# Kernel tuning notes

Hardware: AMD Instinct MI355X
Metric: run time of the kernel (lower is better)

Reference implementation:

```python
import jax, jax.numpy as jnp
import numpy as np

WH, WW = 4, 4
N_TOK = WH * WW  # 16
NUM_HEADS = 8
DIM = 96
HEAD_DIM = DIM // NUM_HEADS
SCALE = HEAD_DIM ** -0.5


def _relative_position_index():
    # Faithful to TF: tf.meshgrid default indexing='xy' (same as np.meshgrid default)
    coords = np.stack(np.meshgrid(np.arange(WH), np.arange(WW)))  # [2, WW, WH]
    flat = coords.reshape(2, -1)                                   # [2, N]
    rel = flat[:, :, None] - flat[:, None, :]                      # [2, N, N]
    rel = rel.transpose(1, 2, 0) + np.array([WH - 1, WW - 1])
    rel = rel * np.array([2 * WW - 1, 1])
    return jnp.asarray(rel.sum(-1), dtype=jnp.int32)               # [N, N]

REL_IDX = _relative_position_index()


def setup_inputs() -> dict:
    key = jax.random.key(0)
    ks = jax.random.split(key, 7)
    B, L = 16, 3136
    return {
        "x": jax.random.normal(ks[0], (B, L, N_TOK, DIM), jnp.float32),
        "mask": jax.random.normal(ks[1], (L, N_TOK, N_TOK), jnp.float32),
        "qkv_kernel": jax.random.normal(ks[2], (DIM, 3 * DIM), jnp.float32) * 0.02,
        "qkv_bias": jax.random.normal(ks[3], (3 * DIM,), jnp.float32) * 0.02,
        "proj_kernel": jax.random.normal(ks[4], (DIM, DIM), jnp.float32) * 0.02,
        "proj_bias": jax.random.normal(ks[5], (DIM,), jnp.float32) * 0.02,
        "bias_table": jax.random.normal(ks[6], (49, NUM_HEADS), jnp.float32) * 0.02,
    }


def reference(x, mask, qkv_kernel, qkv_bias, proj_kernel, proj_bias, bias_table):
    B, L, N, C = x.shape
    H, D = NUM_HEADS, HEAD_DIM
    qkv = x @ qkv_kernel + qkv_bias                      # [B, L, N, 3C]
    qkv = qkv.reshape(B * L, N, 3, H, D).transpose(2, 0, 3, 1, 4)  # [3, BL, H, N, D]
    q, k, v = qkv[0], qkv[1], qkv[2]
    attn = jnp.einsum('whid,whjd->whij', q * SCALE, k)   # [BL, H, N, N]
    rel_bias = bias_table[REL_IDX.reshape(-1)].reshape(N, N, H).transpose(2, 0, 1)  # [H, N, N]
    attn = attn + rel_bias
    attn = attn.reshape(B, L, H, N, N) + mask[:, None, :, :]        # broadcast over B, heads
    attn = jax.nn.softmax(attn.reshape(B * L, H, N, N), axis=-1)
    out = jnp.einsum('whij,whjd->whid', attn, v)         # [BL, H, N, D]
    out = out.transpose(0, 2, 1, 3).reshape(B, L, N, C)
    return out @ proj_kernel + proj_bias
```

## Files before the change

kernel.cpp:

```cpp
#include <hip/hip_runtime.h>


typedef __attribute__((ext_vector_type(4))) float f32x4;
typedef __attribute__((ext_vector_type(8))) short s16x8;
typedef __attribute__((ext_vector_type(4))) short s16x4;

#define DEV __device__ __forceinline__

DEV short f2bf(float f) {
    union { float f; unsigned int i; } v; v.f = f;
    unsigned int u = v.i;
    u += 0x7FFFu + ((u >> 16) & 1u);
    return (short)(u >> 16);
}
DEV void lds_fence() { asm volatile("s_waitcnt lgkmcnt(0)" ::: "memory"); }

#define LOG2E  1.4426950408889634f
#define QSCALE (0.2886751345948129f * 1.4426950408889634f)
#define LBASE  3136
#define WIN_PER_WAVE 49

#define WQ_OFF   0
#define WQ_SZ    (96*288*2)
#define ZP_OFF   WQ_SZ
#define WAVE_BASE (WQ_SZ + 64)
#define PW_Q     0
#define PW_K     4352
#define PW_V     8704
#define PW_A     13312
#define PW_O     23552
#define PW_STRIDE 26880
#define SMEM_TOTAL (WAVE_BASE + 4*PW_STRIDE)

#define MFMA(a,b,c) __builtin_amdgcn_mfma_f32_16x16x32_bf16((a),(b),(c),0,0,0)

__global__ __launch_bounds__(256, 1)
void winattn_kernel(const float* __restrict__ x,
                    const float* __restrict__ mask,
                    const float* __restrict__ qkvK,
                    const float* __restrict__ qkvB,
                    const float* __restrict__ projK,
                    const float* __restrict__ projB,
                    const float* __restrict__ biasT,
                    float* __restrict__ out)
{
    extern __shared__ __align__(16) char smem[];
    const int tid    = threadIdx.x;
    const int lane   = tid & 63;
    const int waveid = tid >> 6;
    const int mi     = lane & 15;
    const int g      = lane >> 4;

    for (int i = tid; i < SMEM_TOTAL/4; i += 256)
        ((unsigned int*)smem)[i] = 0u;
    __syncthreads();

    for (int e = tid; e < 96*288; e += 256) {
        int k = e / 288, n = e % 288;
        int t = n >> 4, mr = n & 15;
        int kt = k >> 5, gg = (k >> 3) & 3, jj = k & 7;
        int gs = gg ^ ((mr >> 1) & 3);
        int off = (t*3 + kt)*512 + mr*32 + gs*8 + jj;
        ((unsigned short*)(smem + WQ_OFF))[off] = (unsigned short)f2bf(qkvK[e]);
    }
    __syncthreads();

    char* wbuf = smem + WAVE_BASE + waveid*PW_STRIDE;
    const char* zp = smem + ZP_OFF;

    s16x8 wp[6][3];
#pragma unroll
    for (int t = 0; t < 6; ++t)
#pragma unroll
        for (int kt = 0; kt < 3; ++kt) {
            s16x8 v;
#pragma unroll
            for (int jj = 0; jj < 8; ++jj)
                v[jj] = f2bf(projK[(kt*32 + g*8 + jj)*96 + t*16 + mi]);
            wp[t][kt] = v;
        }
    f32x4 qb[12];
#pragma unroll
    for (int t = 0; t < 12; ++t) {
        f32x4 v;
#pragma unroll
        for (int r = 0; r < 4; ++r) v[r] = qkvB[t*16 + g*4 + r];
        qb[t] = v;
    }
    float vbias[6];
#pragma unroll
    for (int t = 0; t < 6; ++t) vbias[t] = qkvB[192 + t*16 + mi];
    f32x4 pb[6];
#pragma unroll
    for (int t = 0; t < 6; ++t) {
        f32x4 v;
#pragma unroll
        for (int r = 0; r < 4; ++r) v[r] = projB[t*16 + g*4 + r];
        pb[t] = v;
    }
    f32x4 rb[8];
#pragma unroll
    for (int h = 0; h < 8; ++h) {
        f32x4 v;
#pragma unroll
        for (int r = 0; r < 4; ++r) {
            int i = mi, j = g*4 + r;
            int idx = ((i & 3) - (j & 3) + 3)*7 + ((i >> 2) - (j >> 2) + 3);
            v[r] = biasT[idx*8 + h] * LOG2E;
        }
        rb[h] = v;
    }
    unsigned qkoff[6], voff[6];
#pragma unroll
    for (int t = 0; t < 6; ++t) {
        int f0 = t*16 + g*4;
        qkoff[t] = (unsigned)(mi*272 + (f0/12)*32 + (f0%12)*2);
        int f3 = t*16 + mi;
        voff[t]  = (unsigned)((f3/12)*576 + (f3%12)*48 + g*8);
    }
    const unsigned lane_woff = (unsigned)(mi*64 + ((g ^ ((mi >> 1) & 3)) * 16));

    const int wave_global = blockIdx.x*4 + waveid;
    const int w0 = wave_global * WIN_PER_WAVE;

    f32x4 xa[3], xb[3], mraw;
    {
        const float* xw = x + w0*1536;
#pragma unroll
        for (int kt = 0; kt < 3; ++kt) {
            xa[kt] = *(const f32x4*)(xw + mi*96 + kt*32 + g*8);
            xb[kt] = *(const f32x4*)(xw + mi*96 + kt*32 + g*8 + 4);
        }
        mraw = *(const f32x4*)(mask + (w0 % LBASE)*256 + mi*16 + g*4);
    }

    for (int it = 0; it < WIN_PER_WAVE; ++it) {
        const int w = w0 + it;

        s16x8 xf[3];
#pragma unroll
        for (int kt = 0; kt < 3; ++kt) {
            s16x8 v;
#pragma unroll
            for (int r = 0; r < 4; ++r) { v[r] = f2bf(xa[kt][r]); v[4+r] = f2bf(xb[kt][r]); }
            xf[kt] = v;
        }
        f32x4 mk = mraw;
        mk *= LOG2E;

        {
            const int wn = (it + 1 < WIN_PER_WAVE) ? (w + 1) : w;
            const float* xn = x + wn*1536;
#pragma unroll
            for (int kt = 0; kt < 3; ++kt) {
                xa[kt] = *(const f32x4*)(xn + mi*96 + kt*32 + g*8);
                xb[kt] = *(const f32x4*)(xn + mi*96 + kt*32 + g*8 + 4);
            }
            mraw = *(const f32x4*)(mask + (wn % LBASE)*256 + mi*16 + g*4);
        }

#pragma unroll
        for (int t = 0; t < 12; ++t) {
            f32x4 c = qb[t];
#pragma unroll
            for (int kt = 0; kt < 3; ++kt) {
                s16x8 wf = *(const s16x8*)(smem + WQ_OFF + (t*3 + kt)*1024 + lane_woff);
                c = MFMA(wf, xf[kt], c);
            }
            const float scl = (t < 6) ? QSCALE : 1.0f;
            s16x4 o;
#pragma unroll
            for (int r = 0; r < 4; ++r) o[r] = f2bf(c[r]*scl);
            char* dst = wbuf + ((t < 6) ? PW_Q : PW_K) + qkoff[(t < 6) ? t : (t-6)];
            *(s16x4*)dst = o;
        }
#pragma unroll
        for (int t = 0; t < 6; ++t) {
            f32x4 c = { vbias[t], vbias[t], vbias[t], vbias[t] };
#pragma unroll
            for (int kt = 0; kt < 3; ++kt) {
                s16x8 wf = *(const s16x8*)(smem + WQ_OFF + ((12+t)*3 + kt)*1024 + lane_woff);
                c = MFMA(xf[kt], wf, c);
            }
            s16x4 o;
#pragma unroll
            for (int r = 0; r < 4; ++r) o[r] = f2bf(c[r]);
            *(s16x4*)(wbuf + PW_V + voff[t]) = o;
        }
        lds_fence();

        f32x4 sc[8];
#pragma unroll
        for (int h = 0; h < 8; ++h) {
            const char* qp = (g < 2) ? (wbuf + PW_Q + mi*272 + h*32 + g*16) : zp;
            const char* kp = (g < 2) ? (wbuf + PW_K + mi*272 + h*32 + g*16) : zp;
            s16x8 kf = *(const s16x8*)kp;
            s16x8 qf = *(const s16x8*)qp;
            f32x4 c = rb[h] + mk;
            sc[h] = MFMA(kf, qf, c);
        }
#pragma unroll
        for (int h = 0; h < 8; ++h) {
            float m = fmaxf(fmaxf(sc[h][0], sc[h][1]), fmaxf(sc[h][2], sc[h][3]));
            m = fmaxf(m, __shfl_xor(m, 16, 64));
            m = fmaxf(m, __shfl_xor(m, 32, 64));
            float p0 = exp2f(sc[h][0]-m), p1 = exp2f(sc[h][1]-m),
                  p2 = exp2f(sc[h][2]-m), p3 = exp2f(sc[h][3]-m);
            float s = (p0+p1) + (p2+p3);
            s += __shfl_xor(s, 16, 64);
            s += __shfl_xor(s, 32, 64);
            float rs = 1.0f / s;
            s16x4 av; av[0]=f2bf(p0*rs); av[1]=f2bf(p1*rs); av[2]=f2bf(p2*rs); av[3]=f2bf(p3*rs);
            *(s16x4*)(wbuf + PW_A + h*1280 + mi*80 + g*8) = av;
        }
        lds_fence();

#pragma unroll
        for (int h = 0; h < 8; ++h) {
            s16x8 af = *(const s16x8*)(wbuf + PW_A + h*1280 + mi*80 + g*16);
            const char* vp = (g < 2 && mi < 12) ? (wbuf + PW_V + h*576 + mi*48 + g*16) : zp;
            s16x8 vf = *(const s16x8*)vp;
            f32x4 z = {0.f, 0.f, 0.f, 0.f};
            f32x4 oc = MFMA(vf, af, z);
            if (g < 3) {
                s16x4 ov; ov[0]=f2bf(oc[0]); ov[1]=f2bf(oc[1]); ov[2]=f2bf(oc[2]); ov[3]=f2bf(oc[3]);
                *(s16x4*)(wbuf + PW_O + mi*208 + h*24 + g*8) = ov;
            }
        }
        lds_fence();

        s16x8 of[3];
#pragma unroll
        for (int kt = 0; kt < 3; ++kt)
            of[kt] = *(const s16x8*)(wbuf + PW_O + mi*208 + kt*64 + g*16);
        float* op = out + w*1536 + mi*96 + g*4;
#pragma unroll
        for (int t = 0; t < 6; ++t) {
            f32x4 c = pb[t];
            c = MFMA(wp[t][0], of[0], c);
            c = MFMA(wp[t][1], of[1], c);
            c = MFMA(wp[t][2], of[2], c);
            *(f32x4*)(op + t*16) = c;
        }
    }
}

extern "C" void kernel_launch(void* const* d_in, const int* in_sizes, int n_in,
                              void* d_out, int out_size, void* d_ws, size_t ws_size,
                              hipStream_t stream) {
    const float* x     = (const float*)d_in[0];
    const float* mask  = (const float*)d_in[1];
    const float* qkvK  = (const float*)d_in[2];
    const float* qkvB  = (const float*)d_in[3];
    const float* projK = (const float*)d_in[4];
    const float* projB = (const float*)d_in[5];
    const float* biasT = (const float*)d_in[6];

    (void)in_sizes; (void)n_in; (void)out_size; (void)d_ws; (void)ws_size;

    hipFuncSetAttribute((const void*)winattn_kernel,
                        hipFuncAttributeMaxDynamicSharedMemorySize, SMEM_TOTAL);
    winattn_kernel<<<256, 256, SMEM_TOTAL, stream>>>(
        x, mask, qkvK, qkvB, projK, projB, biasT, (float*)d_out);
}
```

Before: 673.5 us.

## Alias per-wave LDS buffers to run eight waves per block

The per-wave LDS scratch is halved by placing the attention-probability and output staging buffers on top of the Q/K region once scores are computed. This lets each block run 8 waves (512 threads) instead of 4, with windows split fractionally so each wave handles about 24.5 windows. The aim is two waves per SIMD, so MFMA and LDS latency of one wave can hide behind the other. In exchange, padded Q/K columns must be re-zeroed every iteration, the A·V results are buffered in registers before the overwrite, and the 512-thread launch bound with min-blocks 2 tightens the VGPR budget, which risks spills.

```diff
diff --git a/kernel.cpp b/kernel.cpp
--- a/kernel.cpp
+++ b/kernel.cpp
@@ -18,7 +18,6 @@
 #define LOG2E  1.4426950408889634f
 #define QSCALE (0.2886751345948129f * 1.4426950408889634f)
 #define LBASE  3136
-#define WIN_PER_WAVE 49
 
 #define WQ_OFF   0
 #define WQ_SZ    (96*288*2)
@@ -27,14 +26,14 @@
 #define PW_Q     0
 #define PW_K     4352
 #define PW_V     8704
-#define PW_A     13312
-#define PW_O     23552
-#define PW_STRIDE 26880
-#define SMEM_TOTAL (WAVE_BASE + 4*PW_STRIDE)
+#define PW_A     0
+#define PW_O     0
+#define PW_STRIDE 13312
+#define SMEM_TOTAL (WAVE_BASE + 8*PW_STRIDE)
 
 #define MFMA(a,b,c) __builtin_amdgcn_mfma_f32_16x16x32_bf16((a),(b),(c),0,0,0)
 
-__global__ __launch_bounds__(256, 1)
+__global__ __launch_bounds__(512, 2)
 void winattn_kernel(const float* __restrict__ x,
                     const float* __restrict__ mask,
                     const float* __restrict__ qkvK,
@@ -51,11 +50,11 @@
     const int mi     = lane & 15;
     const int g      = lane >> 4;
 
-    for (int i = tid; i < SMEM_TOTAL/4; i += 256)
+    for (int i = tid; i < SMEM_TOTAL/4; i += 512)
         ((unsigned int*)smem)[i] = 0u;
     __syncthreads();
 
-    for (int e = tid; e < 96*288; e += 256) {
+    for (int e = tid; e < 96*288; e += 512) {
         int k = e / 288, n = e % 288;
         int t = n >> 4, mr = n & 15;
         int kt = k >> 5, gg = (k >> 3) & 3, jj = k & 7;
@@ -118,10 +117,14 @@
         int f3 = t*16 + mi;
         voff[t]  = (unsigned)((f3/12)*576 + (f3%12)*48 + g*8);
     }
+    const unsigned pad0 = (unsigned)(mi*272 + g*32 + 24);
+    const unsigned pad1 = (unsigned)(mi*272 + (g+4)*32 + 24);
     const unsigned lane_woff = (unsigned)(mi*64 + ((g ^ ((mi >> 1) & 3)) * 16));
 
-    const int wave_global = blockIdx.x*4 + waveid;
-    const int w0 = wave_global * WIN_PER_WAVE;
+    const int wg = blockIdx.x*8 + waveid;
+    const int w0 = (wg*49) >> 1;
+    const int w1 = ((wg+1)*49) >> 1;
+    const int cnt = w1 - w0;
 
     f32x4 xa[3], xb[3], mraw;
     {
@@ -134,7 +137,7 @@
         mraw = *(const f32x4*)(mask + (w0 % LBASE)*256 + mi*16 + g*4);
     }
 
-    for (int it = 0; it < WIN_PER_WAVE; ++it) {
+    for (int it = 0; it < cnt; ++it) {
         const int w = w0 + it;
 
         s16x8 xf[3];
@@ -149,7 +152,7 @@
         mk *= LOG2E;
 
         {
-            const int wn = (it + 1 < WIN_PER_WAVE) ? (w + 1) : w;
+            const int wn = (it + 1 < cnt) ? (w + 1) : w;
             const float* xn = x + wn*1536;
 #pragma unroll
             for (int kt = 0; kt < 3; ++kt) {
@@ -173,6 +176,13 @@
             for (int r = 0; r < 4; ++r) o[r] = f2bf(c[r]*scl);
             char* dst = wbuf + ((t < 6) ? PW_Q : PW_K) + qkoff[(t < 6) ? t : (t-6)];
             *(s16x4*)dst = o;
+        }
+        {
+            s16x4 zz = {0,0,0,0};
+            *(s16x4*)(wbuf + PW_Q + pad0) = zz;
+            *(s16x4*)(wbuf + PW_Q + pad1) = zz;
+            *(s16x4*)(wbuf + PW_K + pad0) = zz;
+            *(s16x4*)(wbuf + PW_K + pad1) = zz;
         }
 #pragma unroll
         for (int t = 0; t < 6; ++t) {
@@ -211,19 +221,25 @@
             s += __shfl_xor(s, 32, 64);
             float rs = 1.0f / s;
             s16x4 av; av[0]=f2bf(p0*rs); av[1]=f2bf(p1*rs); av[2]=f2bf(p2*rs); av[3]=f2bf(p3*rs);
-            *(s16x4*)(wbuf + PW_A + h*1280 + mi*80 + g*8) = av;
+            *(s16x4*)(wbuf + PW_A + h*768 + mi*48 + g*8) = av;
         }
         lds_fence();
 
-#pragma unroll
-        for (int h = 0; h < 8; ++h) {
-            s16x8 af = *(const s16x8*)(wbuf + PW_A + h*1280 + mi*80 + g*16);
+        f32x4 oc[8];
+#pragma unroll
+        for (int h = 0; h < 8; ++h) {
+            const char* ap = (g < 2) ? (wbuf + PW_A + h*768 + mi*48 + g*16) : zp;
+            s16x8 af = *(const s16x8*)ap;
             const char* vp = (g < 2 && mi < 12) ? (wbuf + PW_V + h*576 + mi*48 + g*16) : zp;
             s16x8 vf = *(const s16x8*)vp;
             f32x4 z = {0.f, 0.f, 0.f, 0.f};
-            f32x4 oc = MFMA(vf, af, z);
+            oc[h] = MFMA(vf, af, z);
+        }
+#pragma unroll
+        for (int h = 0; h < 8; ++h) {
             if (g < 3) {
-                s16x4 ov; ov[0]=f2bf(oc[0]); ov[1]=f2bf(oc[1]); ov[2]=f2bf(oc[2]); ov[3]=f2bf(oc[3]);
+                s16x4 ov; ov[0]=f2bf(oc[h][0]); ov[1]=f2bf(oc[h][1]);
+                          ov[2]=f2bf(oc[h][2]); ov[3]=f2bf(oc[h][3]);
                 *(s16x4*)(wbuf + PW_O + mi*208 + h*24 + g*8) = ov;
             }
         }
@@ -260,6 +276,6 @@
 
     hipFuncSetAttribute((const void*)winattn_kernel,
                         hipFuncAttributeMaxDynamicSharedMemorySize, SMEM_TOTAL);
-    winattn_kernel<<<256, 256, SMEM_TOTAL, stream>>>(
+    winattn_kernel<<<256, 512, SMEM_TOTAL, stream>>>(
         x, mask, qkvK, qkvB, projK, projB, biasT, (float*)d_out);
 }
```

Result: slower. 835.0 us (+24.0%).
